# Kernel optimization log

Measured on AMD Instinct MI355X. Metric: run time of the kernel, lower is better.

The kernel has to match this reference:

```python
import jax, jax.numpy as jnp
import numpy as np

B, N, DIM = 4, 2048, 512
HEADS, DIM_HEAD = 8, 64
INNER = HEADS * DIM_HEAD  # == DIM, so to_out is Identity
LN_EPS = 1e-5
MASK_FILL = 1e-8  # faithful to torch.where(mask, attn, 1e-08)


def setup_inputs() -> dict:
    key = jax.random.key(0)
    k1, k2 = jax.random.split(key)
    x = jax.random.normal(k1, (B, N, DIM), dtype=jnp.float32)
    gamma = jnp.ones((DIM,), dtype=jnp.float32)
    beta = jnp.zeros((DIM,), dtype=jnp.float32)
    w_qkv = jax.random.normal(k2, (3 * INNER, DIM), dtype=jnp.float32) * (DIM ** -0.5)
    mask = jnp.tril(jnp.ones((N, N), dtype=bool))  # causal boolean mask, asserted 2-D in source
    return {"x": x, "gamma": gamma, "beta": beta, "w_qkv": w_qkv, "mask": mask}


def reference(x, gamma, beta, w_qkv, mask):
    # LayerNorm over last dim
    mu = jnp.mean(x, axis=-1, keepdims=True)
    var = jnp.var(x, axis=-1, keepdims=True)
    h = (x - mu) * jax.lax.rsqrt(var + LN_EPS) * gamma + beta
    # qkv projection (no bias), chunk into q, k, v
    qkv = h @ w_qkv.T  # [B, N, 3*INNER]
    q, k, v = jnp.split(qkv, 3, axis=-1)

    def to_heads(t):  # b n (h d) -> b h n d
        return t.reshape(B, N, HEADS, DIM_HEAD).transpose(0, 2, 1, 3)

    q, k, v = to_heads(q), to_heads(k), to_heads(v)
    # NOTE: original forward does NOT apply self.scale
    attn = jnp.einsum('bhnd,bhmd->bhnm', q, k)
    attn = jnp.where(mask[None, None, :, :], attn, MASK_FILL)
    p = jax.nn.softmax(attn, axis=-1)
    out = jnp.einsum('bhnm,bhmd->bhnd', p, v)
    out = out.transpose(0, 2, 1, 3).reshape(B, N, INNER)  # b h n d -> b n (h d)
    return out  # to_out is Identity since INNER == DIM
```

## Files before the change

kernel.cpp:

```cpp
#include <hip/hip_runtime.h>
#include <hip/hip_bf16.h>
#include <math.h>

#define B_  4
#define N_  2048
#define DIM_ 512
#define HEADS_ 8
#define QKV_ 1536
#define MASK_C 1e-8f
#define M_FIX 12.0f
#define LOG2E 1.44269504f

typedef __bf16 bf16_t;
typedef bf16_t bf16x8 __attribute__((ext_vector_type(8)));
typedef float  f32x4  __attribute__((ext_vector_type(4)));

__device__ __forceinline__ bf16_t f2b(float x) { return (bf16_t)x; }
__device__ __forceinline__ float  b2f(bf16_t x) { return (float)x; }

__device__ __forceinline__ f32x4 mfma16(bf16x8 a, bf16x8 b, f32x4 c) {
    return __builtin_amdgcn_mfma_f32_16x16x32_bf16(a, b, c, 0, 0, 0);
}

__global__ __launch_bounds__(256) void ln_wsplit_kernel(const float* __restrict__ x,
                                                        const float* __restrict__ gamma,
                                                        const float* __restrict__ beta,
                                                        bf16_t* __restrict__ hh,
                                                        bf16_t* __restrict__ hl,
                                                        const float* __restrict__ wq,
                                                        bf16_t* __restrict__ wh,
                                                        bf16_t* __restrict__ wl) {
    int blk = blockIdx.x;
    int t = threadIdx.x;
    if (blk >= B_ * N_) {
        int i = ((blk - B_ * N_) * 256 + t) * 4;
        float4 v = *(const float4*)&wq[i];
        float vv[4] = {v.x, v.y, v.z, v.w};
        #pragma unroll
        for (int j = 0; j < 4; j++) {
            bf16_t hi = f2b(vv[j]);
            wh[i + j] = hi;
            wl[i + j] = f2b(vv[j] - b2f(hi));
        }
        return;
    }
    int row = blk;
    const float* xr = x + (size_t)row * DIM_;
    float e0 = xr[t];
    float e1 = xr[t + 256];
    float s  = e0 + e1;
    float sq = e0 * e0 + e1 * e1;
    for (int off = 32; off; off >>= 1) {
        s  += __shfl_xor(s, off);
        sq += __shfl_xor(sq, off);
    }
    __shared__ float red[8];
    int w = t >> 6;
    if ((t & 63) == 0) { red[w] = s; red[4 + w] = sq; }
    __syncthreads();
    float S  = red[0] + red[1] + red[2] + red[3];
    float SQ = red[4] + red[5] + red[6] + red[7];
    float mu = S * (1.0f / DIM_);
    float var = SQ * (1.0f / DIM_) - mu * mu;
    float rs = rsqrtf(var + 1e-5f);
    float y0 = (e0 - mu) * rs * gamma[t] + beta[t];
    float y1 = (e1 - mu) * rs * gamma[t + 256] + beta[t + 256];
    size_t base = (size_t)row * DIM_;
    bf16_t h0 = f2b(y0), h1 = f2b(y1);
    hh[base + t] = h0;       hl[base + t] = f2b(y0 - b2f(h0));
    hh[base + t + 256] = h1; hl[base + t + 256] = f2b(y1 - b2f(h1));
}

__global__ __launch_bounds__(256, 3) void qkv_gemm(const bf16_t* __restrict__ hh,
                                                   const bf16_t* __restrict__ hl,
                                                   const bf16_t* __restrict__ wh,
                                                   const bf16_t* __restrict__ wl,
                                                   bf16_t* __restrict__ qh, bf16_t* __restrict__ ql,
                                                   bf16_t* __restrict__ kh, bf16_t* __restrict__ kl,
                                                   bf16_t* __restrict__ vth,
                                                   float* __restrict__ part) {
    __shared__ __align__(16) bf16_t smem[20480];
    bf16_t* Ah = smem;
    bf16_t* Al = smem + 5120;
    bf16_t* Bh = smem + 10240;
    bf16_t* Bl = smem + 15360;
    int bm = blockIdx.x & 63;
    int bn = blockIdx.x >> 6;
    int t = threadIdx.x;
    int w = t >> 6, lane = t & 63, quad = lane >> 4, l16 = lane & 15;

    f32x4 acc[2][8];
    #pragma unroll
    for (int i = 0; i < 2; i++)
        #pragma unroll
        for (int j = 0; j < 8; j++) acc[i][j] = (f32x4)(0.0f);

    int sr = t >> 1, skc = (t & 1) * 16;
    size_t gA = (size_t)(bm * 128 + sr) * 512 + skc;
    size_t gB = (size_t)(bn * 128 + sr) * 512 + skc;

    uint4 rAh0 = *(const uint4*)&hh[gA];
    uint4 rAh1 = *(const uint4*)&hh[gA + 8];
    uint4 rAl0 = *(const uint4*)&hl[gA];
    uint4 rAl1 = *(const uint4*)&hl[gA + 8];
    uint4 rBh0 = *(const uint4*)&wh[gB];
    uint4 rBh1 = *(const uint4*)&wh[gB + 8];
    uint4 rBl0 = *(const uint4*)&wl[gB];
    uint4 rBl1 = *(const uint4*)&wl[gB + 8];

    for (int k0 = 0; k0 < 512; k0 += 32) {
        __syncthreads();
        *(uint4*)&Ah[sr * 40 + skc]     = rAh0;
        *(uint4*)&Ah[sr * 40 + skc + 8] = rAh1;
        *(uint4*)&Al[sr * 40 + skc]     = rAl0;
        *(uint4*)&Al[sr * 40 + skc + 8] = rAl1;
        *(uint4*)&Bh[sr * 40 + skc]     = rBh0;
        *(uint4*)&Bh[sr * 40 + skc + 8] = rBh1;
        *(uint4*)&Bl[sr * 40 + skc]     = rBl0;
        *(uint4*)&Bl[sr * 40 + skc + 8] = rBl1;
        __syncthreads();

        if (k0 < 480) {
            int kn = k0 + 32;
            rAh0 = *(const uint4*)&hh[gA + kn];
            rAh1 = *(const uint4*)&hh[gA + kn + 8];
            rAl0 = *(const uint4*)&hl[gA + kn];
            rAl1 = *(const uint4*)&hl[gA + kn + 8];
            rBh0 = *(const uint4*)&wh[gB + kn];
            rBh1 = *(const uint4*)&wh[gB + kn + 8];
            rBl0 = *(const uint4*)&wl[gB + kn];
            rBl1 = *(const uint4*)&wl[gB + kn + 8];
        }

        bf16x8 aH[2], aL[2];
        #pragma unroll
        for (int mt = 0; mt < 2; mt++) {
            aH[mt] = *(const bf16x8*)&Ah[(w * 32 + mt * 16 + l16) * 40 + quad * 8];
            aL[mt] = *(const bf16x8*)&Al[(w * 32 + mt * 16 + l16) * 40 + quad * 8];
        }
        #pragma unroll
        for (int nt = 0; nt < 8; nt++) {
            bf16x8 bH = *(const bf16x8*)&Bh[(nt * 16 + l16) * 40 + quad * 8];
            bf16x8 bL = *(const bf16x8*)&Bl[(nt * 16 + l16) * 40 + quad * 8];
            #pragma unroll
            for (int mt = 0; mt < 2; mt++) {
                acc[mt][nt] = mfma16(aH[mt], bH, acc[mt][nt]);
                acc[mt][nt] = mfma16(aH[mt], bL, acc[mt][nt]);
                acc[mt][nt] = mfma16(aL[mt], bH, acc[mt][nt]);
            }
        }
    }

    if (bn < 8) {
        #pragma unroll
        for (int mt = 0; mt < 2; mt++)
            #pragma unroll
            for (int nt = 0; nt < 8; nt++)
                #pragma unroll
                for (int reg = 0; reg < 4; reg++) {
                    float v = acc[mt][nt][reg];
                    int row = bm * 128 + w * 32 + mt * 16 + quad * 4 + reg;
                    int n = bn * 128 + nt * 16 + l16;
                    bf16_t hi = f2b(v);
                    bf16_t lo = f2b(v - b2f(hi));
                    if (n < 512) {
                        size_t a = (size_t)row * 512 + n;
                        qh[a] = hi; ql[a] = lo;
                    } else {
                        size_t a = (size_t)row * 512 + (n - 512);
                        kh[a] = hi; kl[a] = lo;
                    }
                }
    } else {
        int bb = bm >> 4, key0 = (bm & 15) * 128;
        int n = t & 127, mc = (t >> 7) * 64;
        int head = (bn - 8) * 2 + (n >> 6), dd = n & 63;
        size_t obase = ((size_t)((bb * 8 + head) * 64 + dd)) * 2048 + key0 + mc;
        float Ssum = 0.0f;
        #pragma unroll
        for (int pass = 0; pass < 2; pass++) {
            __syncthreads();
            #pragma unroll
            for (int mt = 0; mt < 2; mt++)
                #pragma unroll
                for (int nt = 0; nt < 8; nt++)
                    #pragma unroll
                    for (int reg = 0; reg < 4; reg++) {
                        float v = acc[mt][nt][reg];
                        bf16_t hi = f2b(v);
                        bf16_t val = pass ? f2b(v - b2f(hi)) : hi;
                        smem[(w * 32 + mt * 16 + quad * 4 + reg) * 132 + nt * 16 + l16] = val;
                    }
            __syncthreads();
            #pragma unroll
            for (int i = 0; i < 64; i += 8) {
                __align__(16) bf16_t v8[8];
                #pragma unroll
                for (int j = 0; j < 8; j++) {
                    v8[j] = smem[(mc + i + j) * 132 + n];
                    Ssum += b2f(v8[j]);
                }
                if (pass == 0)
                    *(uint4*)&vth[obase + i] = *(const uint4*)v8;
            }
        }
        int tt = (key0 >> 6) + (mc >> 6);
        part[((size_t)((bb * 8 + head) * 32 + tt)) * 64 + dd] = Ssum;
    }
}

__global__ void vscan_kernel(const float* __restrict__ part,
                             float* __restrict__ suff) {
    int bh = blockIdx.x;
    int d = threadIdx.x;
    float v[32];
    #pragma unroll
    for (int tt = 0; tt < 32; tt++)
        v[tt] = part[((size_t)(bh * 32 + tt)) * 64 + d];
    float S = 0.0f;
    suff[((size_t)bh * 33 + 32) * 64 + d] = 0.0f;
    #pragma unroll
    for (int tt = 31; tt >= 0; tt--) {
        S += v[tt];
        suff[((size_t)bh * 33 + tt) * 64 + d] = S;
    }
}

__global__ __launch_bounds__(256, 2) void attn_kernel(const bf16_t* __restrict__ qh,
                                                      const bf16_t* __restrict__ ql,
                                                      const bf16_t* __restrict__ kh,
                                                      const bf16_t* __restrict__ kl,
                                                      const bf16_t* __restrict__ vth,
                                                      const float* __restrict__ suff,
                                                      float* __restrict__ out) {
    __shared__ __align__(16) bf16_t smem[22016];
    char* lds = (char*)smem;
    bf16_t* Ps = smem + 12288;

    int blk = blockIdx.x;
    int bh = blk & 31;
    int rti = blk >> 5;
    int rt = (rti < 8) ? (15 - rti) : (rti - 8);
    int b = bh >> 3, head = bh & 7;
    int t = threadIdx.x;
    int w = t >> 6, lane = t & 63, quad = lane >> 4, l16 = lane & 15;

    bf16x8 qAH[2][2], qAL[2][2];
    #pragma unroll
    for (int mt = 0; mt < 2; mt++) {
        int qrow = rt * 128 + w * 32 + mt * 16 + l16;
        size_t g = ((size_t)(b * N_ + qrow)) * 512 + head * 64 + quad * 8;
        qAH[mt][0] = *(const bf16x8*)&qh[g];
        qAH[mt][1] = *(const bf16x8*)&qh[g + 32];
        qAL[mt][0] = *(const bf16x8*)&ql[g];
        qAL[mt][1] = *(const bf16x8*)&ql[g + 32];
    }
    bf16x8 ones;
    #pragma unroll
    for (int j = 0; j < 8; j++) ones[j] = f2b(1.0f);

    f32x4 O[2][4];
    #pragma unroll
    for (int mt = 0; mt < 2; mt++)
        #pragma unroll
        for (int nt = 0; nt < 4; nt++) O[mt][nt] = (f32x4)(0.0f);
    f32x4 Lacc[2];
    Lacc[0] = (f32x4)(0.0f); Lacc[1] = (f32x4)(0.0f);
    const float mbias = M_FIX * LOG2E;
    int jmax = 2 * rt + 1;

    int r = t >> 2, c16 = t & 3;
    int swz = (r & 7) << 4;
    int lk0 = r * 128 + ((c16 * 32)      ^ swz);
    int lk1 = r * 128 + ((c16 * 32 + 16) ^ swz);
    size_t gk = ((size_t)(b * N_ + r)) * 512 + head * 64 + c16 * 16;
    size_t gv = ((size_t)(bh * 64 + r)) * 2048 + c16 * 16;

    uint4 pKh0 = *(const uint4*)&kh[gk];
    uint4 pKh1 = *(const uint4*)&kh[gk + 8];
    uint4 pKl0 = *(const uint4*)&kl[gk];
    uint4 pKl1 = *(const uint4*)&kl[gk + 8];
    uint4 pVh0 = *(const uint4*)&vth[gv];
    uint4 pVh1 = *(const uint4*)&vth[gv + 8];

    for (int jt = 0; jt <= jmax; jt++) {
        __syncthreads();
        *(uint4*)(lds + lk0)         = pKh0;
        *(uint4*)(lds + lk1)         = pKh1;
        *(uint4*)(lds + 8192 + lk0)  = pKl0;
        *(uint4*)(lds + 8192 + lk1)  = pKl1;
        *(uint4*)(lds + 16384 + lk0) = pVh0;
        *(uint4*)(lds + 16384 + lk1) = pVh1;
        __syncthreads();

        if (jt < jmax) {
            gk += (size_t)64 * 512;
            gv += 64;
            pKh0 = *(const uint4*)&kh[gk];
            pKh1 = *(const uint4*)&kh[gk + 8];
            pKl0 = *(const uint4*)&kl[gk];
            pKl1 = *(const uint4*)&kl[gk + 8];
            pVh0 = *(const uint4*)&vth[gv];
            pVh1 = *(const uint4*)&vth[gv + 8];
        }

        f32x4 S[2][4];
        #pragma unroll
        for (int mt = 0; mt < 2; mt++)
            #pragma unroll
            for (int nt = 0; nt < 4; nt++) S[mt][nt] = (f32x4)(0.0f);
        #pragma unroll
        for (int khf = 0; khf < 2; khf++) {
            #pragma unroll
            for (int nt = 0; nt < 4; nt++) {
                int row = nt * 16 + l16;
                int bc = (khf * 64 + quad * 16) ^ ((row & 7) << 4);
                bf16x8 bH = *(const bf16x8*)(lds + row * 128 + bc);
                bf16x8 bL = *(const bf16x8*)(lds + 8192 + row * 128 + bc);
                #pragma unroll
                for (int mt = 0; mt < 2; mt++) {
                    S[mt][nt] = mfma16(qAH[mt][khf], bH, S[mt][nt]);
                    S[mt][nt] = mfma16(qAH[mt][khf], bL, S[mt][nt]);
                    S[mt][nt] = mfma16(qAL[mt][khf], bH, S[mt][nt]);
                }
            }
        }

        if (jt >= 2 * rt) {
            #pragma unroll
            for (int mt = 0; mt < 2; mt++) {
                int lrow = rt * 128 + w * 32 + mt * 16 + quad * 4;
                #pragma unroll
                for (int nt = 0; nt < 4; nt++) {
                    int col = jt * 64 + nt * 16 + l16;
                    #pragma unroll
                    for (int reg = 0; reg < 4; reg++)
                        if (col > lrow + reg) S[mt][nt][reg] = MASK_C;
                }
            }
        }

        #pragma unroll
        for (int mt = 0; mt < 2; mt++)
            #pragma unroll
            for (int nt = 0; nt < 4; nt++)
                #pragma unroll
                for (int reg = 0; reg < 4; reg++)
                    Ps[(w * 32 + mt * 16 + quad * 4 + reg) * 76 + nt * 16 + l16] =
                        f2b(exp2f(fmaf(S[mt][nt][reg], LOG2E, -mbias)));

        bf16x8 pH[2][2];
        #pragma unroll
        for (int mt = 0; mt < 2; mt++)
            #pragma unroll
            for (int khf = 0; khf < 2; khf++)
                pH[mt][khf] = *(const bf16x8*)&Ps[(w * 32 + mt * 16 + l16) * 76 +
                                                  khf * 32 + quad * 8];

        #pragma unroll
        for (int mt = 0; mt < 2; mt++)
            #pragma unroll
            for (int khf = 0; khf < 2; khf++)
                Lacc[mt] = mfma16(pH[mt][khf], ones, Lacc[mt]);

        #pragma unroll
        for (int khf = 0; khf < 2; khf++)
            #pragma unroll
            for (int nt = 0; nt < 4; nt++) {
                int row = nt * 16 + l16;
                int bc = (khf * 64 + quad * 16) ^ ((row & 7) << 4);
                bf16x8 vB = *(const bf16x8*)(lds + 16384 + row * 128 + bc);
                #pragma unroll
                for (int mt = 0; mt < 2; mt++)
                    O[mt][nt] = mfma16(pH[mt][khf], vB, O[mt][nt]);
            }
    }

    int ts = 2 * rt + 2;
    int cnt = N_ - ts * 64;
    float L[2][4];
    #pragma unroll
    for (int mt = 0; mt < 2; mt++)
        #pragma unroll
        for (int reg = 0; reg < 4; reg++) L[mt][reg] = Lacc[mt][reg];
    if (cnt > 0) {
        float pc = expf(MASK_C - M_FIX);
        float sv[4];
        #pragma unroll
        for (int nt = 0; nt < 4; nt++)
            sv[nt] = suff[((size_t)bh * 33 + ts) * 64 + nt * 16 + l16];
        #pragma unroll
        for (int mt = 0; mt < 2; mt++)
            #pragma unroll
            for (int reg = 0; reg < 4; reg++) {
                L[mt][reg] += pc * (float)cnt;
                #pragma unroll
                for (int nt = 0; nt < 4; nt++) O[mt][nt][reg] += pc * sv[nt];
            }
    }

    #pragma unroll
    for (int mt = 0; mt < 2; mt++)
        #pragma unroll
        for (int reg = 0; reg < 4; reg++) {
            float rl = 1.0f / L[mt][reg];
            int row = rt * 128 + w * 32 + mt * 16 + quad * 4 + reg;
            #pragma unroll
            for (int nt = 0; nt < 4; nt++)
                out[((size_t)(b * N_ + row)) * DIM_ + head * 64 + nt * 16 + l16] =
                    O[mt][nt][reg] * rl;
        }
}

extern "C" void kernel_launch(void* const* d_in, const int* in_sizes, int n_in,
                              void* d_out, int out_size, void* d_ws, size_t ws_size,
                              hipStream_t stream) {
    const float* x     = (const float*)d_in[0];
    const float* gamma = (const float*)d_in[1];
    const float* beta  = (const float*)d_in[2];
    const float* w_qkv = (const float*)d_in[3];
    float* out = (float*)d_out;

    const size_t HW = (size_t)8192 * 512;
    const size_t WN = (size_t)1536 * 512;
    bf16_t* hh  = (bf16_t*)d_ws;
    bf16_t* hl  = hh + HW;
    bf16_t* qh  = hl + HW;
    bf16_t* ql  = qh + HW;
    bf16_t* kh  = ql + HW;
    bf16_t* kl  = kh + HW;
    bf16_t* vth = kl + HW;
    bf16_t* vtl = vth + HW;
    bf16_t* wh  = vtl + HW;
    bf16_t* wl  = wh + WN;
    float*  part = (float*)(wl + WN);
    float*  suff = part + (size_t)32 * 32 * 64;

    ln_wsplit_kernel<<<B_ * N_ + 768, 256, 0, stream>>>(x, gamma, beta, hh, hl,
                                                        w_qkv, wh, wl);
    qkv_gemm<<<768, 256, 0, stream>>>(hh, hl, wh, wl, qh, ql, kh, kl, vth, part);
    vscan_kernel<<<32, 64, 0, stream>>>(part, suff);
    attn_kernel<<<512, 256, 0, stream>>>(qh, ql, kh, kl, vth, suff, out);
}
```

Before: 203.9 us.

## Vectorize LayerNorm, stage Q/K stores via LDS, double-buffer attention K/V, drop scan kernel

LayerNorm now processes one row per wavefront with float4 loads and 16-byte packed stores, removing the block-level reduction and barrier. Q/K epilogue in the GEMM stages tiles through shared memory to emit coalesced 16-byte stores instead of scattered 2-byte writes. The attention kernel double-buffers K/V tiles in LDS so that only one barrier per iteration is needed, and raises wave priority around MFMA sections. The separate suffix-scan kernel is removed and each attention block sums its own suffix from partial sums, which saves a launch at the cost of extra LDS and some redundant reads.

```diff
diff --git a/kernel.cpp b/kernel.cpp
--- a/kernel.cpp
+++ b/kernel.cpp
@@ -32,8 +32,8 @@
                                                         bf16_t* __restrict__ wl) {
     int blk = blockIdx.x;
     int t = threadIdx.x;
-    if (blk >= B_ * N_) {
-        int i = ((blk - B_ * N_) * 256 + t) * 4;
+    if (blk >= 2048) {
+        int i = ((blk - 2048) * 256 + t) * 4;
         float4 v = *(const float4*)&wq[i];
         float vv[4] = {v.x, v.y, v.z, v.w};
         #pragma unroll
@@ -44,31 +44,39 @@
         }
         return;
     }
-    int row = blk;
+    int w = t >> 6, lane = t & 63;
+    int row = blk * 4 + w;
     const float* xr = x + (size_t)row * DIM_;
-    float e0 = xr[t];
-    float e1 = xr[t + 256];
-    float s  = e0 + e1;
-    float sq = e0 * e0 + e1 * e1;
+    float4 a = *(const float4*)&xr[lane * 8];
+    float4 c = *(const float4*)&xr[lane * 8 + 4];
+    float e[8] = {a.x, a.y, a.z, a.w, c.x, c.y, c.z, c.w};
+    float s = 0.0f, sq = 0.0f;
+    #pragma unroll
+    for (int j = 0; j < 8; j++) { s += e[j]; sq += e[j] * e[j]; }
     for (int off = 32; off; off >>= 1) {
         s  += __shfl_xor(s, off);
         sq += __shfl_xor(sq, off);
     }
-    __shared__ float red[8];
-    int w = t >> 6;
-    if ((t & 63) == 0) { red[w] = s; red[4 + w] = sq; }
-    __syncthreads();
-    float S  = red[0] + red[1] + red[2] + red[3];
-    float SQ = red[4] + red[5] + red[6] + red[7];
-    float mu = S * (1.0f / DIM_);
-    float var = SQ * (1.0f / DIM_) - mu * mu;
+    float mu = s * (1.0f / DIM_);
+    float var = sq * (1.0f / DIM_) - mu * mu;
     float rs = rsqrtf(var + 1e-5f);
-    float y0 = (e0 - mu) * rs * gamma[t] + beta[t];
-    float y1 = (e1 - mu) * rs * gamma[t + 256] + beta[t + 256];
-    size_t base = (size_t)row * DIM_;
-    bf16_t h0 = f2b(y0), h1 = f2b(y1);
-    hh[base + t] = h0;       hl[base + t] = f2b(y0 - b2f(h0));
-    hh[base + t + 256] = h1; hl[base + t + 256] = f2b(y1 - b2f(h1));
+    float4 g0 = *(const float4*)&gamma[lane * 8];
+    float4 g1 = *(const float4*)&gamma[lane * 8 + 4];
+    float4 b0 = *(const float4*)&beta[lane * 8];
+    float4 b1 = *(const float4*)&beta[lane * 8 + 4];
+    float gm[8] = {g0.x, g0.y, g0.z, g0.w, g1.x, g1.y, g1.z, g1.w};
+    float bt[8] = {b0.x, b0.y, b0.z, b0.w, b1.x, b1.y, b1.z, b1.w};
+    __align__(16) bf16_t hp[8], lp[8];
+    #pragma unroll
+    for (int j = 0; j < 8; j++) {
+        float y = (e[j] - mu) * rs * gm[j] + bt[j];
+        bf16_t hi = f2b(y);
+        hp[j] = hi;
+        lp[j] = f2b(y - b2f(hi));
+    }
+    size_t base = (size_t)row * DIM_ + lane * 8;
+    *(uint4*)&hh[base] = *(const uint4*)hp;
+    *(uint4*)&hl[base] = *(const uint4*)lp;
 }
 
 __global__ __launch_bounds__(256, 3) void qkv_gemm(const bf16_t* __restrict__ hh,
@@ -152,31 +160,10 @@
     }
 
     if (bn < 8) {
-        #pragma unroll
-        for (int mt = 0; mt < 2; mt++)
-            #pragma unroll
-            for (int nt = 0; nt < 8; nt++)
-                #pragma unroll
-                for (int reg = 0; reg < 4; reg++) {
-                    float v = acc[mt][nt][reg];
-                    int row = bm * 128 + w * 32 + mt * 16 + quad * 4 + reg;
-                    int n = bn * 128 + nt * 16 + l16;
-                    bf16_t hi = f2b(v);
-                    bf16_t lo = f2b(v - b2f(hi));
-                    if (n < 512) {
-                        size_t a = (size_t)row * 512 + n;
-                        qh[a] = hi; ql[a] = lo;
-                    } else {
-                        size_t a = (size_t)row * 512 + (n - 512);
-                        kh[a] = hi; kl[a] = lo;
-                    }
-                }
-    } else {
-        int bb = bm >> 4, key0 = (bm & 15) * 128;
-        int n = t & 127, mc = (t >> 7) * 64;
-        int head = (bn - 8) * 2 + (n >> 6), dd = n & 63;
-        size_t obase = ((size_t)((bb * 8 + head) * 64 + dd)) * 2048 + key0 + mc;
-        float Ssum = 0.0f;
+        bf16_t* dsth = (bn < 4) ? qh : kh;
+        bf16_t* dstl = (bn < 4) ? ql : kl;
+        int ncol0 = (bn & 3) * 128 + (t & 15) * 8;
+        int r0 = t >> 4;
         #pragma unroll
         for (int pass = 0; pass < 2; pass++) {
             __syncthreads();
@@ -192,6 +179,35 @@
                         smem[(w * 32 + mt * 16 + quad * 4 + reg) * 132 + nt * 16 + l16] = val;
                     }
             __syncthreads();
+            bf16_t* dst = pass ? dstl : dsth;
+            #pragma unroll
+            for (int i = 0; i < 8; i++) {
+                int row = r0 + i * 16;
+                *(uint4*)&dst[(size_t)(bm * 128 + row) * 512 + ncol0] =
+                    *(const uint4*)&smem[row * 132 + ((t & 15) * 8)];
+            }
+        }
+    } else {
+        int bb = bm >> 4, key0 = (bm & 15) * 128;
+        int n = t & 127, mc = (t >> 7) * 64;
+        int head = (bn - 8) * 2 + (n >> 6), dd = n & 63;
+        size_t obase = ((size_t)((bb * 8 + head) * 64 + dd)) * 2048 + key0 + mc;
+        float Ssum = 0.0f;
+        #pragma unroll
+        for (int pass = 0; pass < 2; pass++) {
+            __syncthreads();
+            #pragma unroll
+            for (int mt = 0; mt < 2; mt++)
+                #pragma unroll
+                for (int nt = 0; nt < 8; nt++)
+                    #pragma unroll
+                    for (int reg = 0; reg < 4; reg++) {
+                        float v = acc[mt][nt][reg];
+                        bf16_t hi = f2b(v);
+                        bf16_t val = pass ? f2b(v - b2f(hi)) : hi;
+                        smem[(w * 32 + mt * 16 + quad * 4 + reg) * 132 + nt * 16 + l16] = val;
+                    }
+            __syncthreads();
             #pragma unroll
             for (int i = 0; i < 64; i += 8) {
                 __align__(16) bf16_t v8[8];
@@ -209,41 +225,34 @@
     }
 }
 
-__global__ void vscan_kernel(const float* __restrict__ part,
-                             float* __restrict__ suff) {
-    int bh = blockIdx.x;
-    int d = threadIdx.x;
-    float v[32];
-    #pragma unroll
-    for (int tt = 0; tt < 32; tt++)
-        v[tt] = part[((size_t)(bh * 32 + tt)) * 64 + d];
-    float S = 0.0f;
-    suff[((size_t)bh * 33 + 32) * 64 + d] = 0.0f;
-    #pragma unroll
-    for (int tt = 31; tt >= 0; tt--) {
-        S += v[tt];
-        suff[((size_t)bh * 33 + tt) * 64 + d] = S;
-    }
-}
-
 __global__ __launch_bounds__(256, 2) void attn_kernel(const bf16_t* __restrict__ qh,
                                                       const bf16_t* __restrict__ ql,
                                                       const bf16_t* __restrict__ kh,
                                                       const bf16_t* __restrict__ kl,
                                                       const bf16_t* __restrict__ vth,
-                                                      const float* __restrict__ suff,
+                                                      const float* __restrict__ part,
                                                       float* __restrict__ out) {
-    __shared__ __align__(16) bf16_t smem[22016];
+    __shared__ __align__(16) bf16_t smem[24576];
+    __shared__ __align__(16) bf16_t Ps[4 * 32 * 76];
+    __shared__ float sufl[4][64];
     char* lds = (char*)smem;
-    bf16_t* Ps = smem + 12288;
 
     int blk = blockIdx.x;
     int bh = blk & 31;
-    int rti = blk >> 5;
-    int rt = (rti < 8) ? (15 - rti) : (rti - 8);
+    int gi = blk >> 5;
+    int rt = (gi < 8) ? (15 - gi) : (gi - 8);
     int b = bh >> 3, head = bh & 7;
     int t = threadIdx.x;
     int w = t >> 6, lane = t & 63, quad = lane >> 4, l16 = lane & 15;
+    int jmax = 2 * rt + 1;
+
+    {
+        int d = t & 63, g = t >> 6;
+        float s = 0.0f;
+        for (int tt = jmax + 1 + g; tt < 32; tt += 4)
+            s += part[((size_t)bh * 32 + tt) * 64 + d];
+        sufl[g][d] = s;
+    }
 
     bf16x8 qAH[2][2], qAL[2][2];
     #pragma unroll
@@ -267,7 +276,6 @@
     f32x4 Lacc[2];
     Lacc[0] = (f32x4)(0.0f); Lacc[1] = (f32x4)(0.0f);
     const float mbias = M_FIX * LOG2E;
-    int jmax = 2 * rt + 1;
 
     int r = t >> 2, c16 = t & 3;
     int swz = (r & 7) << 4;
@@ -282,16 +290,17 @@
     uint4 pKl1 = *(const uint4*)&kl[gk + 8];
     uint4 pVh0 = *(const uint4*)&vth[gv];
     uint4 pVh1 = *(const uint4*)&vth[gv + 8];
+    *(uint4*)(lds + lk0)         = pKh0;
+    *(uint4*)(lds + lk1)         = pKh1;
+    *(uint4*)(lds + 8192 + lk0)  = pKl0;
+    *(uint4*)(lds + 8192 + lk1)  = pKl1;
+    *(uint4*)(lds + 16384 + lk0) = pVh0;
+    *(uint4*)(lds + 16384 + lk1) = pVh1;
+    __syncthreads();
 
     for (int jt = 0; jt <= jmax; jt++) {
-        __syncthreads();
-        *(uint4*)(lds + lk0)         = pKh0;
-        *(uint4*)(lds + lk1)         = pKh1;
-        *(uint4*)(lds + 8192 + lk0)  = pKl0;
-        *(uint4*)(lds + 8192 + lk1)  = pKl1;
-        *(uint4*)(lds + 16384 + lk0) = pVh0;
-        *(uint4*)(lds + 16384 + lk1) = pVh1;
-        __syncthreads();
+        char* cur = lds + (jt & 1) * 24576;
+        char* nxt = lds + ((jt + 1) & 1) * 24576;
 
         if (jt < jmax) {
             gk += (size_t)64 * 512;
@@ -309,14 +318,15 @@
         for (int mt = 0; mt < 2; mt++)
             #pragma unroll
             for (int nt = 0; nt < 4; nt++) S[mt][nt] = (f32x4)(0.0f);
+        __builtin_amdgcn_s_setprio(1);
         #pragma unroll
         for (int khf = 0; khf < 2; khf++) {
             #pragma unroll
             for (int nt = 0; nt < 4; nt++) {
                 int row = nt * 16 + l16;
                 int bc = (khf * 64 + quad * 16) ^ ((row & 7) << 4);
-                bf16x8 bH = *(const bf16x8*)(lds + row * 128 + bc);
-                bf16x8 bL = *(const bf16x8*)(lds + 8192 + row * 128 + bc);
+                bf16x8 bH = *(const bf16x8*)(cur + row * 128 + bc);
+                bf16x8 bL = *(const bf16x8*)(cur + 8192 + row * 128 + bc);
                 #pragma unroll
                 for (int mt = 0; mt < 2; mt++) {
                     S[mt][nt] = mfma16(qAH[mt][khf], bH, S[mt][nt]);
@@ -325,6 +335,7 @@
                 }
             }
         }
+        __builtin_amdgcn_s_setprio(0);
 
         if (jt >= 2 * rt) {
             #pragma unroll
@@ -357,6 +368,7 @@
                 pH[mt][khf] = *(const bf16x8*)&Ps[(w * 32 + mt * 16 + l16) * 76 +
                                                   khf * 32 + quad * 8];
 
+        __builtin_amdgcn_s_setprio(1);
         #pragma unroll
         for (int mt = 0; mt < 2; mt++)
             #pragma unroll
@@ -369,11 +381,22 @@
             for (int nt = 0; nt < 4; nt++) {
                 int row = nt * 16 + l16;
                 int bc = (khf * 64 + quad * 16) ^ ((row & 7) << 4);
-                bf16x8 vB = *(const bf16x8*)(lds + 16384 + row * 128 + bc);
+                bf16x8 vB = *(const bf16x8*)(cur + 16384 + row * 128 + bc);
                 #pragma unroll
                 for (int mt = 0; mt < 2; mt++)
                     O[mt][nt] = mfma16(pH[mt][khf], vB, O[mt][nt]);
             }
+        __builtin_amdgcn_s_setprio(0);
+
+        if (jt < jmax) {
+            *(uint4*)(nxt + lk0)         = pKh0;
+            *(uint4*)(nxt + lk1)         = pKh1;
+            *(uint4*)(nxt + 8192 + lk0)  = pKl0;
+            *(uint4*)(nxt + 8192 + lk1)  = pKl1;
+            *(uint4*)(nxt + 16384 + lk0) = pVh0;
+            *(uint4*)(nxt + 16384 + lk1) = pVh1;
+        }
+        __syncthreads();
     }
 
     int ts = 2 * rt + 2;
@@ -387,8 +410,10 @@
         float pc = expf(MASK_C - M_FIX);
         float sv[4];
         #pragma unroll
-        for (int nt = 0; nt < 4; nt++)
-            sv[nt] = suff[((size_t)bh * 33 + ts) * 64 + nt * 16 + l16];
+        for (int nt = 0; nt < 4; nt++) {
+            int d = nt * 16 + l16;
+            sv[nt] = sufl[0][d] + sufl[1][d] + sufl[2][d] + sufl[3][d];
+        }
         #pragma unroll
         for (int mt = 0; mt < 2; mt++)
             #pragma unroll
@@ -434,11 +459,9 @@
     bf16_t* wh  = vtl + HW;
     bf16_t* wl  = wh + WN;
     float*  part = (float*)(wl + WN);
-    float*  suff = part + (size_t)32 * 32 * 64;
-
-    ln_wsplit_kernel<<<B_ * N_ + 768, 256, 0, stream>>>(x, gamma, beta, hh, hl,
-                                                        w_qkv, wh, wl);
+
+    ln_wsplit_kernel<<<2048 + 768, 256, 0, stream>>>(x, gamma, beta, hh, hl,
+                                                     w_qkv, wh, wl);
     qkv_gemm<<<768, 256, 0, stream>>>(hh, hl, wh, wl, qh, ql, kh, kl, vth, part);
-    vscan_kernel<<<32, 64, 0, stream>>>(part, suff);
-    attn_kernel<<<512, 256, 0, stream>>>(qh, ql, kh, kl, vth, suff, out);
+    attn_kernel<<<512, 256, 0, stream>>>(qh, ql, kh, kl, vth, part, out);
 }
```

New measurement: 201.9 us. About the same (-1.0%).
